# Performance work log

Measured on AMD Instinct MI355X. Metric: run time of the kernel, lower is better.

## Reference

```python
import jax, jax.numpy as jnp
import numpy as np

INPUT, UNITS, MOTOR, OUT = 1, 256, 64, 32
REM = UNITS - MOTOR
COMMAND = max(int(0.4 * REM), 1)   # 76
INTER = REM - COMMAND              # 116
B, L = 512, 1024
DIMS = [(INPUT, INTER), (INTER, COMMAND), (COMMAND, MOTOR)]


def setup_inputs() -> dict:
    rng = np.random.default_rng(0)
    inp = {}
    inp['dt'] = jnp.asarray(rng.random((B, L, INPUT)).astype(np.float32))
    inp['hx'] = jnp.asarray(rng.standard_normal((B, UNITS)).astype(np.float32))
    for i, (din, h) in enumerate(DIMS):
        c = din + h
        s = 1.0 / np.sqrt(c)
        for nm in ('W1', 'W2', 'Wa', 'Wb'):
            inp[f'l{i}_{nm}'] = jnp.asarray((rng.standard_normal((h, c)) * s).astype(np.float32))
        for nm in ('b1', 'b2', 'ba', 'bb'):
            inp[f'l{i}_{nm}'] = jnp.asarray((rng.standard_normal((h,)) * s).astype(np.float32))
        # NCP sparsity mask: random cross-layer connectivity (density ~0.5), dense recurrent block
        cross = (rng.random((h, din)) < 0.5).astype(np.int32)
        rec = np.ones((h, h), dtype=np.int32)
        inp[f'mask{i}'] = jnp.asarray(np.concatenate([cross, rec], axis=1))
    so = 1.0 / np.sqrt(MOTOR)
    inp['Wout'] = jnp.asarray((rng.standard_normal((OUT, MOTOR)) * so).astype(np.float32))
    inp['bout'] = jnp.asarray((rng.standard_normal((OUT,)) * so).astype(np.float32))
    return inp


def _cfc_cell(x, W1, W2, Wa, Wb, b1, b2, ba, bb, mask):
    # CfC 'default' mode, ts = 1.0 (CfC called without timespans; dt is the input signal)
    m = mask.astype(x.dtype)
    ff1 = jnp.tanh(x @ (W1 * m).T + b1)
    ff2 = jnp.tanh(x @ (W2 * m).T + b2)
    t_interp = jax.nn.sigmoid((x @ Wa.T + ba) + (x @ Wb.T + bb))
    return ff1 * (1.0 - t_interp) + t_interp * ff2


def _forward(dt, hx, params, masks, Wout, bout):
    # hx layout follows WiredCfCCell layer order: [inter, command, motor]
    h0, h1, h2 = jnp.split(hx, [INTER, INTER + COMMAND], axis=1)

    def step(carry, dt_t):
        h0, h1, h2 = carry
        h0 = _cfc_cell(jnp.concatenate([dt_t, h0], axis=-1), *params[0], masks[0])
        h1 = _cfc_cell(jnp.concatenate([h0, h1], axis=-1), *params[1], masks[1])
        h2 = _cfc_cell(jnp.concatenate([h1, h2], axis=-1), *params[2], masks[2])
        return (h0, h1, h2), h2

    _, ys = jax.lax.scan(step, (h0, h1, h2), jnp.swapaxes(dt, 0, 1))  # (L, B, MOTOR)
    readout = jnp.swapaxes(ys, 0, 1)  # (B, L, MOTOR)
    return readout @ Wout.T + bout    # (B, L, OUT)


def reference(dt, hx, l0_W1, l0_W2, l0_Wa, l0_Wb, l0_b1, l0_b2, l0_ba, l0_bb, l1_W1, l1_W2, l1_Wa, l1_Wb, l1_b1, l1_b2, l1_ba, l1_bb, l2_W1, l2_W2, l2_Wa, l2_Wb, l2_b1, l2_b2, l2_ba, l2_bb, mask0, mask1, mask2, Wout, bout):
    params = [
        (l0_W1, l0_W2, l0_Wa, l0_Wb, l0_b1, l0_b2, l0_ba, l0_bb),
        (l1_W1, l1_W2, l1_Wa, l1_Wb, l1_b1, l1_b2, l1_ba, l1_bb),
        (l2_W1, l2_W2, l2_Wa, l2_Wb, l2_b1, l2_b2, l2_ba, l2_bb),
    ]
    return _forward(dt, hx, params, (mask0, mask1, mask2), Wout, bout)
```

## Files before the change

### kernel.cpp

```cpp
#include <hip/hip_runtime.h>
#include <stdint.h>

typedef _Float16 f16;
typedef _Float16 h2v __attribute__((ext_vector_type(2)));
typedef _Float16 F16x4 __attribute__((ext_vector_type(4)));
typedef _Float16 F16x8 __attribute__((ext_vector_type(8)));
typedef float F32x4 __attribute__((ext_vector_type(4)));

#define MFMA16(a,b,c) __builtin_amdgcn_mfma_f32_16x16x32_f16((a),(b),(c),0,0,0)
#define S12f 2.8853900817779268f
#define SABf (-1.4426950408889634f)

static __device__ __forceinline__ float exp2f_b(float x){ return __builtin_amdgcn_exp2f(x); }

static __device__ __forceinline__ f16 cfc_act3(float p1,float p2,float ps){
  float E1=exp2f_b(p1), E2=exp2f_b(p2), es=exp2f_b(ps);
  float t1=E1+1.f, u=(E2+1.f)*(1.f+es);
  float num=u-(E2-E1);
  float r=__builtin_amdgcn_rcpf(t1*u);
  return (f16)(1.f-2.f*num*r);
}
static __device__ __forceinline__ int fidx(int k,int b){ return ((k>>3)<<7)+(b<<3)+(k&7); }

static __device__ __forceinline__ void tick_barrier(){
  asm volatile("s_waitcnt lgkmcnt(0)" ::: "memory");
  __builtin_amdgcn_s_barrier();
}

__global__ __launch_bounds__(256) void cfc_prep(
    const float* __restrict__ W10,const float* __restrict__ W20,const float* __restrict__ Wa0,const float* __restrict__ Wb0,
    const float* __restrict__ b10,const float* __restrict__ b20,const float* __restrict__ ba0,const float* __restrict__ bb0,
    const int* __restrict__ M0,
    const float* __restrict__ W11,const float* __restrict__ W21,const float* __restrict__ Wa1,const float* __restrict__ Wb1,
    const float* __restrict__ b11,const float* __restrict__ b21,const float* __restrict__ ba1,const float* __restrict__ bb1,
    const int* __restrict__ M1,
    const float* __restrict__ W12,const float* __restrict__ W22,const float* __restrict__ Wa2,const float* __restrict__ Wb2,
    const float* __restrict__ b12,const float* __restrict__ b22,const float* __restrict__ ba2,const float* __restrict__ bb2,
    const int* __restrict__ M2,
    const float* __restrict__ Wo, f16* __restrict__ ws)
{
  int idx=blockIdx.x*256+threadIdx.x;
  if(idx>=16704) return;
  int tile=idx>>6, lane=idx&63, ml=lane&15, grp=lane>>4;
  int lay,nb,m,kt,c,h;
  const float *w1,*w2,*wa,*wb,*c1,*c2,*ca,*cb; const int* M;
  if(tile<96){ lay=0; int u=tile; kt=u&3; int q=u>>2; m=q%3; nb=q/3; c=117; h=116;
    w1=W10;w2=W20;wa=Wa0;wb=Wb0;M=M0;c1=b10;c2=b20;ca=ba0;cb=bb0; }
  else if(tile<201){ lay=1; int u=tile-96; kt=u%7; int q=u/7; m=q%3; nb=q/3; c=192; h=76;
    w1=W11;w2=W21;wa=Wa1;wb=Wb1;M=M1;c1=b11;c2=b21;ca=ba1;cb=bb1; }
  else { lay=2; int u=tile-201; kt=u%5; int q=u/5; m=q%3; nb=q/3; c=140; h=64;
    w1=W12;w2=W22;wa=Wa2;wb=Wb2;M=M2;c1=b12;c2=b22;ca=ba2;cb=bb2; }
  int n=nb*16+ml;
  float sc=(m<2)?S12f:SABf;
  int k0=kt*32+grp*8;
  F16x8 fr;
  #pragma unroll
  for(int j=0;j<8;++j){
    int k=k0+j; float v=0.f; int col=-1;
    if(lay==0){       if(k<116) col=1+k; else if(k==124) col=0; else if(k==125) col=-2; }
    else if(lay==1){  if(k<116) col=k; else if(k>=128 && k<204) col=116+(k-128); else if(k==125) col=-2; }
    else {            if(k<76) col=k; else if(k>=96 && k<160) col=76+(k-96); else if(k==88) col=-2; }
    if(n<h){
      if(col>=0){
        if(m==0){ v=w1[n*c+col]*(float)M[n*c+col]; }
        else if(m==1){ v=w2[n*c+col]*(float)M[n*c+col]; }
        else { v=wa[n*c+col]+wb[n*c+col]; }
      } else if(col==-2){
        v=(m==0)?c1[n]:(m==1)?c2[n]:(ca[n]+cb[n]);
      }
    }
    fr[j]=(f16)(v*sc);
  }
  ((F16x8*)ws)[idx]=fr;
}

__global__ __launch_bounds__(1024,4) void cfc_main(
    const float* __restrict__ dtp, const float* __restrict__ hxp,
    const f16* __restrict__ ws, float* __restrict__ outp)
{
  const int tid=threadIdx.x, lane=tid&63, w=tid>>6;
  const int b_l=lane&15, g_l=lane>>4;
  const int gb0=blockIdx.x*16;

  __shared__ alignas(16) f16 H0[2][2048];
  __shared__ alignas(16) f16 H1[2][1536];
  __shared__ alignas(16) f16 H2[2][1024];
  __shared__ f16 DTS[16448];

  const F16x8* wsf=(const F16x8*)ws;
  F32x4 ZED; ZED[0]=0.f; ZED[1]=0.f; ZED[2]=0.f; ZED[3]=0.f;

  for(int i=tid;i<4096;i+=1024) ((f16*)H0)[i]=(f16)0.f;
  for(int i=tid;i<3072;i+=1024) ((f16*)H1)[i]=(f16)0.f;
  for(int i=tid;i<2048;i+=1024) ((f16*)H2)[i]=(f16)0.f;
  for(int i=tid;i<16448;i+=1024){
    int t=i>>4, b=i&15;
    DTS[i]=(t<1024)?(f16)dtp[(size_t)(gb0+b)*1024+t]:(f16)0.f;
  }
  __syncthreads();
  for(int i=tid;i<4096;i+=1024){ int b=i>>8,u=i&255; f16 v=(f16)hxp[(size_t)(gb0+b)*256+u];
    if(u<116){ H0[0][fidx(u,b)]=v; H0[1][fidx(u,b)]=v; }
    else if(u<192){ int n=u-116; H1[0][fidx(n,b)]=v; H1[1][fidx(n,b)]=v; }
    else { int n=u-192; H2[0][fidx(n,b)]=v; H2[1][fidx(n,b)]=v; }
  }
  if(tid<16){
    H0[1][fidx(124,tid)]=DTS[tid];
    H0[0][fidx(125,tid)]=(f16)1.f; H0[1][fidx(125,tid)]=(f16)1.f;
    H1[0][fidx(88,tid)]=(f16)1.f;  H1[1][fidx(88,tid)]=(f16)1.f;
  }
  __syncthreads();

  int type, nb=0;
  if(w==0){ type=0; }
  else if(w==1){type=1;nb=0;} else if(w==5){type=1;nb=1;} else if(w==2){type=1;nb=2;}
  else if(w==3){type=1;nb=3;} else if(w==7){type=1;nb=4;}
  else if(w==4){type=3;nb=0;} else if(w==6){type=3;nb=1;} else if(w==10){type=3;nb=2;}
  else { type=2; nb=(w==8)?0:(w==12)?1:(w==9)?2:(w==13)?3:(w==14)?4:(w==11)?5:6; }

  if(type==0){
    F16x8 wm0[3][4], wm2[3][5];
    #pragma unroll
    for(int m=0;m<3;++m){
      #pragma unroll
      for(int kt=0;kt<4;++kt) wm0[m][kt]=wsf[((7*3+m)*4+kt)*64+lane];
      #pragma unroll
      for(int kt=0;kt<5;++kt) wm2[m][kt]=wsf[(201+(3*3+m)*5+kt)*64+lane];
    }
    const int wk0=fidx(112+g_l*4,b_l);
    const int wk2=fidx(48+g_l*4,b_l);
#define MG_TICK(I_,P_) do{ \
      if((I_)<=1023){ \
        F16x8 Af0=((const F16x8*)H0[(P_)^1])[0*64+lane]; \
        F16x8 Af1=((const F16x8*)H0[(P_)^1])[1*64+lane]; \
        F16x8 Af2=((const F16x8*)H0[(P_)^1])[2*64+lane]; \
        F16x8 Af3=((const F16x8*)H0[(P_)^1])[3*64+lane]; \
        F32x4 a0=MFMA16(wm0[0][0],Af0,ZED), a1=MFMA16(wm0[1][0],Af0,ZED), a2=MFMA16(wm0[2][0],Af0,ZED); \
        a0=MFMA16(wm0[0][1],Af1,a0); a1=MFMA16(wm0[1][1],Af1,a1); a2=MFMA16(wm0[2][1],Af1,a2); \
        a0=MFMA16(wm0[0][2],Af2,a0); a1=MFMA16(wm0[1][2],Af2,a1); a2=MFMA16(wm0[2][2],Af2,a2); \
        a0=MFMA16(wm0[0][3],Af3,a0); a1=MFMA16(wm0[1][3],Af3,a1); a2=MFMA16(wm0[2][3],Af3,a2); \
        if(g_l==0){ \
          F16x4 v; v[0]=cfc_act3(a0[0],a1[0],a2[0]); v[1]=cfc_act3(a0[1],a1[1],a2[1]); \
          v[2]=cfc_act3(a0[2],a1[2],a2[2]); v[3]=cfc_act3(a0[3],a1[3],a2[3]); \
          *(F16x4*)&H0[P_][wk0]=v; } \
      } \
      if((I_)>=2 && (I_)<=1025){ \
        F16x8 Cf0=((const F16x8*)H1[(P_)^1])[0*64+lane]; \
        F16x8 Cf1=((const F16x8*)H1[(P_)^1])[1*64+lane]; \
        F16x8 Cf2=((const F16x8*)H1[(P_)^1])[2*64+lane]; \
        F16x8 Cf3=((const F16x8*)H2[(P_)^1])[0*64+lane]; \
        F16x8 Cf4=((const F16x8*)H2[(P_)^1])[1*64+lane]; \
        F32x4 c0=MFMA16(wm2[0][0],Cf0,ZED), c1=MFMA16(wm2[1][0],Cf0,ZED), c2=MFMA16(wm2[2][0],Cf0,ZED); \
        c0=MFMA16(wm2[0][1],Cf1,c0); c1=MFMA16(wm2[1][1],Cf1,c1); c2=MFMA16(wm2[2][1],Cf1,c2); \
        c0=MFMA16(wm2[0][2],Cf2,c0); c1=MFMA16(wm2[1][2],Cf2,c1); c2=MFMA16(wm2[2][2],Cf2,c2); \
        c0=MFMA16(wm2[0][3],Cf3,c0); c1=MFMA16(wm2[1][3],Cf3,c1); c2=MFMA16(wm2[2][3],Cf3,c2); \
        c0=MFMA16(wm2[0][4],Cf4,c0); c1=MFMA16(wm2[1][4],Cf4,c1); c2=MFMA16(wm2[2][4],Cf4,c2); \
        F16x4 v; v[0]=cfc_act3(c0[0],c1[0],c2[0]); v[1]=cfc_act3(c0[1],c1[1],c2[1]); \
        v[2]=cfc_act3(c0[2],c1[2],c2[2]); v[3]=cfc_act3(c0[3],c1[3],c2[3]); \
        *(F16x4*)&H2[P_][wk2]=v; \
      } }while(0)
    for(int I2=0;I2<1028;I2+=2){
      MG_TICK(I2,0);   tick_barrier();
      MG_TICK(I2+1,1); tick_barrier();
    }
#undef MG_TICK
  } else if(type==1){
    F16x8 wf[3][7];
    #pragma unroll
    for(int m=0;m<3;++m)
      #pragma unroll
      for(int kt=0;kt<7;++kt) wf[m][kt]=wsf[(96+(nb*3+m)*7+kt)*64+lane];
    const int wk=fidx(nb*16+g_l*4,b_l);
    const bool wr_ok=(nb<4)||(g_l<3);
#define L1_TICK(I_,P_) do{ \
      if((I_)>=1 && (I_)<=1024){ \
        F16x8 Af0=((const F16x8*)H0[(P_)^1])[0*64+lane]; \
        F16x8 Af1=((const F16x8*)H0[(P_)^1])[1*64+lane]; \
        F16x8 Af2=((const F16x8*)H0[(P_)^1])[2*64+lane]; \
        F16x8 Af3=((const F16x8*)H0[(P_)^1])[3*64+lane]; \
        F16x8 Hf0=((const F16x8*)H1[(P_)^1])[0*64+lane]; \
        F16x8 Hf1=((const F16x8*)H1[(P_)^1])[1*64+lane]; \
        F16x8 Hf2=((const F16x8*)H1[(P_)^1])[2*64+lane]; \
        F32x4 a0=MFMA16(wf[0][0],Af0,ZED), a1=MFMA16(wf[1][0],Af0,ZED), a2=MFMA16(wf[2][0],Af0,ZED); \
        a0=MFMA16(wf[0][1],Af1,a0); a1=MFMA16(wf[1][1],Af1,a1); a2=MFMA16(wf[2][1],Af1,a2); \
        a0=MFMA16(wf[0][2],Af2,a0); a1=MFMA16(wf[1][2],Af2,a1); a2=MFMA16(wf[2][2],Af2,a2); \
        a0=MFMA16(wf[0][3],Af3,a0); a1=MFMA16(wf[1][3],Af3,a1); a2=MFMA16(wf[2][3],Af3,a2); \
        a0=MFMA16(wf[0][4],Hf0,a0); a1=MFMA16(wf[1][4],Hf0,a1); a2=MFMA16(wf[2][4],Hf0,a2); \
        a0=MFMA16(wf[0][5],Hf1,a0); a1=MFMA16(wf[1][5],Hf1,a1); a2=MFMA16(wf[2][5],Hf1,a2); \
        a0=MFMA16(wf[0][6],Hf2,a0); a1=MFMA16(wf[1][6],Hf2,a1); a2=MFMA16(wf[2][6],Hf2,a2); \
        F16x4 v; v[0]=cfc_act3(a0[0],a1[0],a2[0]); v[1]=cfc_act3(a0[1],a1[1],a2[1]); \
        v[2]=cfc_act3(a0[2],a1[2],a2[2]); v[3]=cfc_act3(a0[3],a1[3],a2[3]); \
        if(wr_ok) *(F16x4*)&H1[P_][wk]=v; \
      } }while(0)
    for(int I2=0;I2<1028;I2+=2){
      L1_TICK(I2,0);   tick_barrier();
      L1_TICK(I2+1,1); tick_barrier();
    }
#undef L1_TICK
  } else if(type==2){
    F16x8 wf[3][4];
    #pragma unroll
    for(int m=0;m<3;++m)
      #pragma unroll
      for(int kt=0;kt<4;++kt) wf[m][kt]=wsf[((nb*3+m)*4+kt)*64+lane];
    const int wk=fidx(nb*16+g_l*4,b_l);
    const bool dost=(w==9)||(w==14);
    const int q=lane&7, bb=(lane>>3)+8*((w==9)?0:1);
    char* outPtr=(char*)outp + ((size_t)(gb0+bb)*1024)*128 + q*16;
#define L0_TICK(I_,P_) do{ \
      if((I_)<=1023){ \
        F16x8 Af0=((const F16x8*)H0[(P_)^1])[0*64+lane]; \
        F16x8 Af1=((const F16x8*)H0[(P_)^1])[1*64+lane]; \
        F16x8 Af2=((const F16x8*)H0[(P_)^1])[2*64+lane]; \
        F16x8 Af3=((const F16x8*)H0[(P_)^1])[3*64+lane]; \
        F32x4 a0=MFMA16(wf[0][0],Af0,ZED), a1=MFMA16(wf[1][0],Af0,ZED), a2=MFMA16(wf[2][0],Af0,ZED); \
        a0=MFMA16(wf[0][1],Af1,a0); a1=MFMA16(wf[1][1],Af1,a1); a2=MFMA16(wf[2][1],Af1,a2); \
        a0=MFMA16(wf[0][2],Af2,a0); a1=MFMA16(wf[1][2],Af2,a1); a2=MFMA16(wf[2][2],Af2,a2); \
        a0=MFMA16(wf[0][3],Af3,a0); a1=MFMA16(wf[1][3],Af3,a1); a2=MFMA16(wf[2][3],Af3,a2); \
        F16x4 v; v[0]=cfc_act3(a0[0],a1[0],a2[0]); v[1]=cfc_act3(a0[1],a1[1],a2[1]); \
        v[2]=cfc_act3(a0[2],a1[2],a2[2]); v[3]=cfc_act3(a0[3],a1[3],a2[3]); \
        *(F16x4*)&H0[P_][wk]=v; \
      } \
      if(dost && (I_)>=3 && (I_)<=1026){ \
        F16x8 sv=((const F16x8*)H2[(P_)^1])[q*16+bb]; \
        *(F16x8*)outPtr=sv; outPtr+=128; \
      } }while(0)
    for(int I2=0;I2<1028;I2+=2){
      L0_TICK(I2,0);   tick_barrier();
      L0_TICK(I2+1,1); tick_barrier();
    }
#undef L0_TICK
  } else {
    F16x8 wf[3][5];
    #pragma unroll
    for(int m=0;m<3;++m)
      #pragma unroll
      for(int kt=0;kt<5;++kt) wf[m][kt]=wsf[(201+(nb*3+m)*5+kt)*64+lane];
    const int wk=fidx(nb*16+g_l*4,b_l);
    const bool dodt=(w==6);
#define L2_TICK(I_,P_) do{ \
      if(dodt && lane<16 && (I_)<=1022) H0[P_][fidx(124,lane)]=DTS[((I_)+1)*16+lane]; \
      if((I_)>=2 && (I_)<=1025){ \
        F16x8 Cf0=((const F16x8*)H1[(P_)^1])[0*64+lane]; \
        F16x8 Cf1=((const F16x8*)H1[(P_)^1])[1*64+lane]; \
        F16x8 Cf2=((const F16x8*)H1[(P_)^1])[2*64+lane]; \
        F16x8 Cf3=((const F16x8*)H2[(P_)^1])[0*64+lane]; \
        F16x8 Cf4=((const F16x8*)H2[(P_)^1])[1*64+lane]; \
        F32x4 a0=MFMA16(wf[0][0],Cf0,ZED), a1=MFMA16(wf[1][0],Cf0,ZED), a2=MFMA16(wf[2][0],Cf0,ZED); \
        a0=MFMA16(wf[0][1],Cf1,a0); a1=MFMA16(wf[1][1],Cf1,a1); a2=MFMA16(wf[2][1],Cf1,a2); \
        a0=MFMA16(wf[0][2],Cf2,a0); a1=MFMA16(wf[1][2],Cf2,a1); a2=MFMA16(wf[2][2],Cf2,a2); \
        a0=MFMA16(wf[0][3],Cf3,a0); a1=MFMA16(wf[1][3],Cf3,a1); a2=MFMA16(wf[2][3],Cf3,a2); \
        a0=MFMA16(wf[0][4],Cf4,a0); a1=MFMA16(wf[1][4],Cf4,a1); a2=MFMA16(wf[2][4],Cf4,a2); \
        F16x4 v; v[0]=cfc_act3(a0[0],a1[0],a2[0]); v[1]=cfc_act3(a0[1],a1[1],a2[1]); \
        v[2]=cfc_act3(a0[2],a1[2],a2[2]); v[3]=cfc_act3(a0[3],a1[3],a2[3]); \
        *(F16x4*)&H2[P_][wk]=v; \
      } }while(0)
    for(int I2=0;I2<1028;I2+=2){
      L2_TICK(I2,0);   tick_barrier();
      L2_TICK(I2+1,1); tick_barrier();
    }
#undef L2_TICK
  }
}

__global__ __launch_bounds__(256) void cfc_ro(
    const float* __restrict__ Wo, const float* __restrict__ bo, float* __restrict__ outp)
{
  __shared__ h2v wT[1024];
  __shared__ float bs[32];
  int tid=threadIdx.x;
  for(int i=tid;i<1024;i+=256){ int kp=i>>5,o=i&31;
    h2v v; v[0]=(f16)Wo[o*64+2*kp]; v[1]=(f16)Wo[o*64+2*kp+1]; wT[i]=v; }
  if(tid<32) bs[tid]=bo[tid];
  __syncthreads();
  size_t s=(size_t)blockIdx.x*256+tid;
  float* slot=outp+s*32;
  h2v x[32];
  #pragma unroll
  for(int r=0;r<8;++r) ((F16x8*)x)[r]=((const F16x8*)slot)[r];
  float y[32];
  #pragma unroll
  for(int o=0;o<32;++o){
    float acc=bs[o];
    #pragma unroll
    for(int kp=0;kp<32;++kp) acc=__builtin_amdgcn_fdot2(x[kp],wT[kp*32+o],acc,false);
    y[o]=acc;
  }
  #pragma unroll
  for(int r=0;r<8;++r) ((float4*)slot)[r]=((const float4*)y)[r];
}

extern "C" void kernel_launch(void* const* d_in, const int* in_sizes, int n_in,
                              void* d_out, int out_size, void* d_ws, size_t ws_size,
                              hipStream_t stream)
{
  (void)in_sizes; (void)n_in; (void)out_size; (void)ws_size;
  f16* ws=(f16*)d_ws;
  cfc_prep<<<66,256,0,stream>>>(
    (const float*)d_in[2],(const float*)d_in[3],(const float*)d_in[4],(const float*)d_in[5],
    (const float*)d_in[6],(const float*)d_in[7],(const float*)d_in[8],(const float*)d_in[9],
    (const int*)d_in[10],
    (const float*)d_in[11],(const float*)d_in[12],(const float*)d_in[13],(const float*)d_in[14],
    (const float*)d_in[15],(const float*)d_in[16],(const float*)d_in[17],(const float*)d_in[18],
    (const int*)d_in[19],
    (const float*)d_in[20],(const float*)d_in[21],(const float*)d_in[22],(const float*)d_in[23],
    (const float*)d_in[24],(const float*)d_in[25],(const float*)d_in[26],(const float*)d_in[27],
    (const int*)d_in[28],
    (const float*)d_in[29], ws);
  cfc_main<<<32,1024,0,stream>>>(
    (const float*)d_in[0],(const float*)d_in[1], ws, (float*)d_out);
  cfc_ro<<<2048,256,0,stream>>>(
    (const float*)d_in[29],(const float*)d_in[30],(float*)d_out);
}
```

Before: 1.040 ms.

## Halve workgroup to 8 waves, each computing multiple output blocks per tick

The recurrent kernel moves from 16 waves per block to 8 waves, and the per-layer work is reassigned. Most waves now compute two or three 16-row output blocks per timestep, reusing the same loaded activation fragments across more MFMA chains. Fewer waves cut the cost of the two barriers per step and the redundant LDS fragment reads. In exchange, each wave has a longer serial MFMA and activation chain per tick and holds more weight registers, which may lengthen the critical path of each step.

Result: slower. 1.073 ms (+3.1%).

```diff
diff --git a/kernel.cpp b/kernel.cpp
--- a/kernel.cpp
+++ b/kernel.cpp
@@ -19,6 +19,12 @@
   float num=u-(E2-E1);
   float r=__builtin_amdgcn_rcpf(t1*u);
   return (f16)(1.f-2.f*num*r);
+}
+static __device__ __forceinline__ F16x4 pack_act3(F32x4 a0,F32x4 a1,F32x4 a2){
+  F16x4 v;
+  v[0]=cfc_act3(a0[0],a1[0],a2[0]); v[1]=cfc_act3(a0[1],a1[1],a2[1]);
+  v[2]=cfc_act3(a0[2],a1[2],a2[2]); v[3]=cfc_act3(a0[3],a1[3],a2[3]);
+  return v;
 }
 static __device__ __forceinline__ int fidx(int k,int b){ return ((k>>3)<<7)+(b<<3)+(k&7); }
 
@@ -74,7 +80,7 @@
   ((F16x8*)ws)[idx]=fr;
 }
 
-__global__ __launch_bounds__(1024,4) void cfc_main(
+__global__ __launch_bounds__(512,2) void cfc_main(
     const float* __restrict__ dtp, const float* __restrict__ hxp,
     const f16* __restrict__ ws, float* __restrict__ outp)
 {
@@ -90,15 +96,15 @@
   const F16x8* wsf=(const F16x8*)ws;
   F32x4 ZED; ZED[0]=0.f; ZED[1]=0.f; ZED[2]=0.f; ZED[3]=0.f;
 
-  for(int i=tid;i<4096;i+=1024) ((f16*)H0)[i]=(f16)0.f;
-  for(int i=tid;i<3072;i+=1024) ((f16*)H1)[i]=(f16)0.f;
-  for(int i=tid;i<2048;i+=1024) ((f16*)H2)[i]=(f16)0.f;
-  for(int i=tid;i<16448;i+=1024){
+  for(int i=tid;i<4096;i+=512) ((f16*)H0)[i]=(f16)0.f;
+  for(int i=tid;i<3072;i+=512) ((f16*)H1)[i]=(f16)0.f;
+  for(int i=tid;i<2048;i+=512) ((f16*)H2)[i]=(f16)0.f;
+  for(int i=tid;i<16448;i+=512){
     int t=i>>4, b=i&15;
     DTS[i]=(t<1024)?(f16)dtp[(size_t)(gb0+b)*1024+t]:(f16)0.f;
   }
   __syncthreads();
-  for(int i=tid;i<4096;i+=1024){ int b=i>>8,u=i&255; f16 v=(f16)hxp[(size_t)(gb0+b)*256+u];
+  for(int i=tid;i<4096;i+=512){ int b=i>>8,u=i&255; f16 v=(f16)hxp[(size_t)(gb0+b)*256+u];
     if(u<116){ H0[0][fidx(u,b)]=v; H0[1][fidx(u,b)]=v; }
     else if(u<192){ int n=u-116; H1[0][fidx(n,b)]=v; H1[1][fidx(n,b)]=v; }
     else { int n=u-192; H2[0][fidx(n,b)]=v; H2[1][fidx(n,b)]=v; }
@@ -110,68 +116,17 @@
   }
   __syncthreads();
 
-  int type, nb=0;
-  if(w==0){ type=0; }
-  else if(w==1){type=1;nb=0;} else if(w==5){type=1;nb=1;} else if(w==2){type=1;nb=2;}
-  else if(w==3){type=1;nb=3;} else if(w==7){type=1;nb=4;}
-  else if(w==4){type=3;nb=0;} else if(w==6){type=3;nb=1;} else if(w==10){type=3;nb=2;}
-  else { type=2; nb=(w==8)?0:(w==12)?1:(w==9)?2:(w==13)?3:(w==14)?4:(w==11)?5:6; }
-
-  if(type==0){
-    F16x8 wm0[3][4], wm2[3][5];
-    #pragma unroll
-    for(int m=0;m<3;++m){
-      #pragma unroll
-      for(int kt=0;kt<4;++kt) wm0[m][kt]=wsf[((7*3+m)*4+kt)*64+lane];
-      #pragma unroll
-      for(int kt=0;kt<5;++kt) wm2[m][kt]=wsf[(201+(3*3+m)*5+kt)*64+lane];
-    }
-    const int wk0=fidx(112+g_l*4,b_l);
-    const int wk2=fidx(48+g_l*4,b_l);
-#define MG_TICK(I_,P_) do{ \
-      if((I_)<=1023){ \
-        F16x8 Af0=((const F16x8*)H0[(P_)^1])[0*64+lane]; \
-        F16x8 Af1=((const F16x8*)H0[(P_)^1])[1*64+lane]; \
-        F16x8 Af2=((const F16x8*)H0[(P_)^1])[2*64+lane]; \
-        F16x8 Af3=((const F16x8*)H0[(P_)^1])[3*64+lane]; \
-        F32x4 a0=MFMA16(wm0[0][0],Af0,ZED), a1=MFMA16(wm0[1][0],Af0,ZED), a2=MFMA16(wm0[2][0],Af0,ZED); \
-        a0=MFMA16(wm0[0][1],Af1,a0); a1=MFMA16(wm0[1][1],Af1,a1); a2=MFMA16(wm0[2][1],Af1,a2); \
-        a0=MFMA16(wm0[0][2],Af2,a0); a1=MFMA16(wm0[1][2],Af2,a1); a2=MFMA16(wm0[2][2],Af2,a2); \
-        a0=MFMA16(wm0[0][3],Af3,a0); a1=MFMA16(wm0[1][3],Af3,a1); a2=MFMA16(wm0[2][3],Af3,a2); \
-        if(g_l==0){ \
-          F16x4 v; v[0]=cfc_act3(a0[0],a1[0],a2[0]); v[1]=cfc_act3(a0[1],a1[1],a2[1]); \
-          v[2]=cfc_act3(a0[2],a1[2],a2[2]); v[3]=cfc_act3(a0[3],a1[3],a2[3]); \
-          *(F16x4*)&H0[P_][wk0]=v; } \
-      } \
-      if((I_)>=2 && (I_)<=1025){ \
-        F16x8 Cf0=((const F16x8*)H1[(P_)^1])[0*64+lane]; \
-        F16x8 Cf1=((const F16x8*)H1[(P_)^1])[1*64+lane]; \
-        F16x8 Cf2=((const F16x8*)H1[(P_)^1])[2*64+lane]; \
-        F16x8 Cf3=((const F16x8*)H2[(P_)^1])[0*64+lane]; \
-        F16x8 Cf4=((const F16x8*)H2[(P_)^1])[1*64+lane]; \
-        F32x4 c0=MFMA16(wm2[0][0],Cf0,ZED), c1=MFMA16(wm2[1][0],Cf0,ZED), c2=MFMA16(wm2[2][0],Cf0,ZED); \
-        c0=MFMA16(wm2[0][1],Cf1,c0); c1=MFMA16(wm2[1][1],Cf1,c1); c2=MFMA16(wm2[2][1],Cf1,c2); \
-        c0=MFMA16(wm2[0][2],Cf2,c0); c1=MFMA16(wm2[1][2],Cf2,c1); c2=MFMA16(wm2[2][2],Cf2,c2); \
-        c0=MFMA16(wm2[0][3],Cf3,c0); c1=MFMA16(wm2[1][3],Cf3,c1); c2=MFMA16(wm2[2][3],Cf3,c2); \
-        c0=MFMA16(wm2[0][4],Cf4,c0); c1=MFMA16(wm2[1][4],Cf4,c1); c2=MFMA16(wm2[2][4],Cf4,c2); \
-        F16x4 v; v[0]=cfc_act3(c0[0],c1[0],c2[0]); v[1]=cfc_act3(c0[1],c1[1],c2[1]); \
-        v[2]=cfc_act3(c0[2],c1[2],c2[2]); v[3]=cfc_act3(c0[3],c1[3],c2[3]); \
-        *(F16x4*)&H2[P_][wk2]=v; \
-      } }while(0)
-    for(int I2=0;I2<1028;I2+=2){
-      MG_TICK(I2,0);   tick_barrier();
-      MG_TICK(I2+1,1); tick_barrier();
-    }
-#undef MG_TICK
-  } else if(type==1){
-    F16x8 wf[3][7];
-    #pragma unroll
-    for(int m=0;m<3;++m)
-      #pragma unroll
-      for(int kt=0;kt<7;++kt) wf[m][kt]=wsf[(96+(nb*3+m)*7+kt)*64+lane];
-    const int wk=fidx(nb*16+g_l*4,b_l);
-    const bool wr_ok=(nb<4)||(g_l<3);
-#define L1_TICK(I_,P_) do{ \
+  if(w<2){
+    const int NB=2*w;
+    F16x8 wf[6][7];
+    #pragma unroll
+    for(int u=0;u<2;++u)
+      #pragma unroll
+      for(int m=0;m<3;++m)
+        #pragma unroll
+        for(int kt=0;kt<7;++kt) wf[u*3+m][kt]=wsf[(96+((NB+u)*3+m)*7+kt)*64+lane];
+    const int wka=fidx((NB+0)*16+g_l*4,b_l), wkb=fidx((NB+1)*16+g_l*4,b_l);
+#define L1P_TICK(I_,P_) do{ \
       if((I_)>=1 && (I_)<=1024){ \
         F16x8 Af0=((const F16x8*)H0[(P_)^1])[0*64+lane]; \
         F16x8 Af1=((const F16x8*)H0[(P_)^1])[1*64+lane]; \
@@ -181,33 +136,44 @@
         F16x8 Hf1=((const F16x8*)H1[(P_)^1])[1*64+lane]; \
         F16x8 Hf2=((const F16x8*)H1[(P_)^1])[2*64+lane]; \
         F32x4 a0=MFMA16(wf[0][0],Af0,ZED), a1=MFMA16(wf[1][0],Af0,ZED), a2=MFMA16(wf[2][0],Af0,ZED); \
+        F32x4 b0=MFMA16(wf[3][0],Af0,ZED), b1=MFMA16(wf[4][0],Af0,ZED), b2=MFMA16(wf[5][0],Af0,ZED); \
         a0=MFMA16(wf[0][1],Af1,a0); a1=MFMA16(wf[1][1],Af1,a1); a2=MFMA16(wf[2][1],Af1,a2); \
+        b0=MFMA16(wf[3][1],Af1,b0); b1=MFMA16(wf[4][1],Af1,b1); b2=MFMA16(wf[5][1],Af1,b2); \
         a0=MFMA16(wf[0][2],Af2,a0); a1=MFMA16(wf[1][2],Af2,a1); a2=MFMA16(wf[2][2],Af2,a2); \
+        b0=MFMA16(wf[3][2],Af2,b0); b1=MFMA16(wf[4][2],Af2,b1); b2=MFMA16(wf[5][2],Af2,b2); \
         a0=MFMA16(wf[0][3],Af3,a0); a1=MFMA16(wf[1][3],Af3,a1); a2=MFMA16(wf[2][3],Af3,a2); \
+        b0=MFMA16(wf[3][3],Af3,b0); b1=MFMA16(wf[4][3],Af3,b1); b2=MFMA16(wf[5][3],Af3,b2); \
         a0=MFMA16(wf[0][4],Hf0,a0); a1=MFMA16(wf[1][4],Hf0,a1); a2=MFMA16(wf[2][4],Hf0,a2); \
+        b0=MFMA16(wf[3][4],Hf0,b0); b1=MFMA16(wf[4][4],Hf0,b1); b2=MFMA16(wf[5][4],Hf0,b2); \
         a0=MFMA16(wf[0][5],Hf1,a0); a1=MFMA16(wf[1][5],Hf1,a1); a2=MFMA16(wf[2][5],Hf1,a2); \
+        b0=MFMA16(wf[3][5],Hf1,b0); b1=MFMA16(wf[4][5],Hf1,b1); b2=MFMA16(wf[5][5],Hf1,b2); \
         a0=MFMA16(wf[0][6],Hf2,a0); a1=MFMA16(wf[1][6],Hf2,a1); a2=MFMA16(wf[2][6],Hf2,a2); \
-        F16x4 v; v[0]=cfc_act3(a0[0],a1[0],a2[0]); v[1]=cfc_act3(a0[1],a1[1],a2[1]); \
-        v[2]=cfc_act3(a0[2],a1[2],a2[2]); v[3]=cfc_act3(a0[3],a1[3],a2[3]); \
-        if(wr_ok) *(F16x4*)&H1[P_][wk]=v; \
+        b0=MFMA16(wf[3][6],Hf2,b0); b1=MFMA16(wf[4][6],Hf2,b1); b2=MFMA16(wf[5][6],Hf2,b2); \
+        *(F16x4*)&H1[P_][wka]=pack_act3(a0,a1,a2); \
+        *(F16x4*)&H1[P_][wkb]=pack_act3(b0,b1,b2); \
       } }while(0)
     for(int I2=0;I2<1028;I2+=2){
-      L1_TICK(I2,0);   tick_barrier();
-      L1_TICK(I2+1,1); tick_barrier();
-    }
-#undef L1_TICK
-  } else if(type==2){
-    F16x8 wf[3][4];
-    #pragma unroll
-    for(int m=0;m<3;++m)
-      #pragma unroll
-      for(int kt=0;kt<4;++kt) wf[m][kt]=wsf[((nb*3+m)*4+kt)*64+lane];
-    const int wk=fidx(nb*16+g_l*4,b_l);
-    const bool dost=(w==9)||(w==14);
-    const int q=lane&7, bb=(lane>>3)+8*((w==9)?0:1);
-    char* outPtr=(char*)outp + ((size_t)(gb0+bb)*1024)*128 + q*16;
-#define L0_TICK(I_,P_) do{ \
-      if((I_)<=1023){ \
+      L1P_TICK(I2,0);   tick_barrier();
+      L1P_TICK(I2+1,1); tick_barrier();
+    }
+#undef L1P_TICK
+  } else if(w==2){
+    F16x8 wf[3][7], wc[3][5];
+    #pragma unroll
+    for(int m=0;m<3;++m){
+      #pragma unroll
+      for(int kt=0;kt<7;++kt) wf[m][kt]=wsf[(96+(4*3+m)*7+kt)*64+lane];
+      #pragma unroll
+      for(int kt=0;kt<5;++kt) wc[m][kt]=wsf[(201+(0*3+m)*5+kt)*64+lane];
+    }
+    const int wk1=fidx(64+g_l*4,b_l);
+    const int wk2=fidx(0+g_l*4,b_l);
+    const bool wr1=(g_l<3);
+#define MIX_TICK(I_,P_) do{ \
+      F16x8 Hf0=((const F16x8*)H1[(P_)^1])[0*64+lane]; \
+      F16x8 Hf1=((const F16x8*)H1[(P_)^1])[1*64+lane]; \
+      F16x8 Hf2=((const F16x8*)H1[(P_)^1])[2*64+lane]; \
+      if((I_)>=1 && (I_)<=1024){ \
         F16x8 Af0=((const F16x8*)H0[(P_)^1])[0*64+lane]; \
         F16x8 Af1=((const F16x8*)H0[(P_)^1])[1*64+lane]; \
         F16x8 Af2=((const F16x8*)H0[(P_)^1])[2*64+lane]; \
@@ -216,49 +182,109 @@
         a0=MFMA16(wf[0][1],Af1,a0); a1=MFMA16(wf[1][1],Af1,a1); a2=MFMA16(wf[2][1],Af1,a2); \
         a0=MFMA16(wf[0][2],Af2,a0); a1=MFMA16(wf[1][2],Af2,a1); a2=MFMA16(wf[2][2],Af2,a2); \
         a0=MFMA16(wf[0][3],Af3,a0); a1=MFMA16(wf[1][3],Af3,a1); a2=MFMA16(wf[2][3],Af3,a2); \
-        F16x4 v; v[0]=cfc_act3(a0[0],a1[0],a2[0]); v[1]=cfc_act3(a0[1],a1[1],a2[1]); \
-        v[2]=cfc_act3(a0[2],a1[2],a2[2]); v[3]=cfc_act3(a0[3],a1[3],a2[3]); \
-        *(F16x4*)&H0[P_][wk]=v; \
+        a0=MFMA16(wf[0][4],Hf0,a0); a1=MFMA16(wf[1][4],Hf0,a1); a2=MFMA16(wf[2][4],Hf0,a2); \
+        a0=MFMA16(wf[0][5],Hf1,a0); a1=MFMA16(wf[1][5],Hf1,a1); a2=MFMA16(wf[2][5],Hf1,a2); \
+        a0=MFMA16(wf[0][6],Hf2,a0); a1=MFMA16(wf[1][6],Hf2,a1); a2=MFMA16(wf[2][6],Hf2,a2); \
+        F16x4 v=pack_act3(a0,a1,a2); \
+        if(wr1) *(F16x4*)&H1[P_][wk1]=v; \
+      } \
+      if((I_)>=2 && (I_)<=1025){ \
+        F16x8 Gf0=((const F16x8*)H2[(P_)^1])[0*64+lane]; \
+        F16x8 Gf1=((const F16x8*)H2[(P_)^1])[1*64+lane]; \
+        F32x4 c0=MFMA16(wc[0][0],Hf0,ZED), c1=MFMA16(wc[1][0],Hf0,ZED), c2=MFMA16(wc[2][0],Hf0,ZED); \
+        c0=MFMA16(wc[0][1],Hf1,c0); c1=MFMA16(wc[1][1],Hf1,c1); c2=MFMA16(wc[2][1],Hf1,c2); \
+        c0=MFMA16(wc[0][2],Hf2,c0); c1=MFMA16(wc[1][2],Hf2,c1); c2=MFMA16(wc[2][2],Hf2,c2); \
+        c0=MFMA16(wc[0][3],Gf0,c0); c1=MFMA16(wc[1][3],Gf0,c1); c2=MFMA16(wc[2][3],Gf0,c2); \
+        c0=MFMA16(wc[0][4],Gf1,c0); c1=MFMA16(wc[1][4],Gf1,c1); c2=MFMA16(wc[2][4],Gf1,c2); \
+        *(F16x4*)&H2[P_][wk2]=pack_act3(c0,c1,c2); \
+      } }while(0)
+    for(int I2=0;I2<1028;I2+=2){
+      MIX_TICK(I2,0);   tick_barrier();
+      MIX_TICK(I2+1,1); tick_barrier();
+    }
+#undef MIX_TICK
+  } else if(w==3){
+    F16x8 wc[9][5];
+    #pragma unroll
+    for(int u=0;u<3;++u)
+      #pragma unroll
+      for(int m=0;m<3;++m)
+        #pragma unroll
+        for(int kt=0;kt<5;++kt) wc[u*3+m][kt]=wsf[(201+((1+u)*3+m)*5+kt)*64+lane];
+    const int wka=fidx(16+g_l*4,b_l), wkb=fidx(32+g_l*4,b_l), wkc=fidx(48+g_l*4,b_l);
+#define L2T_TICK(I_,P_) do{ \
+      if((I_)>=2 && (I_)<=1025){ \
+        F16x8 Hf0=((const F16x8*)H1[(P_)^1])[0*64+lane]; \
+        F16x8 Hf1=((const F16x8*)H1[(P_)^1])[1*64+lane]; \
+        F16x8 Hf2=((const F16x8*)H1[(P_)^1])[2*64+lane]; \
+        F16x8 Gf0=((const F16x8*)H2[(P_)^1])[0*64+lane]; \
+        F16x8 Gf1=((const F16x8*)H2[(P_)^1])[1*64+lane]; \
+        F32x4 a0=MFMA16(wc[0][0],Hf0,ZED), a1=MFMA16(wc[1][0],Hf0,ZED), a2=MFMA16(wc[2][0],Hf0,ZED); \
+        F32x4 b0=MFMA16(wc[3][0],Hf0,ZED), b1=MFMA16(wc[4][0],Hf0,ZED), b2=MFMA16(wc[5][0],Hf0,ZED); \
+        F32x4 c0=MFMA16(wc[6][0],Hf0,ZED), c1=MFMA16(wc[7][0],Hf0,ZED), c2=MFMA16(wc[8][0],Hf0,ZED); \
+        a0=MFMA16(wc[0][1],Hf1,a0); a1=MFMA16(wc[1][1],Hf1,a1); a2=MFMA16(wc[2][1],Hf1,a2); \
+        b0=MFMA16(wc[3][1],Hf1,b0); b1=MFMA16(wc[4][1],Hf1,b1); b2=MFMA16(wc[5][1],Hf1,b2); \
+        c0=MFMA16(wc[6][1],Hf1,c0); c1=MFMA16(wc[7][1],Hf1,c1); c2=MFMA16(wc[8][1],Hf1,c2); \
+        a0=MFMA16(wc[0][2],Hf2,a0); a1=MFMA16(wc[1][2],Hf2,a1); a2=MFMA16(wc[2][2],Hf2,a2); \
+        b0=MFMA16(wc[3][2],Hf2,b0); b1=MFMA16(wc[4][2],Hf2,b1); b2=MFMA16(wc[5][2],Hf2,b2); \
+        c0=MFMA16(wc[6][2],Hf2,c0); c1=MFMA16(wc[7][2],Hf2,c1); c2=MFMA16(wc[8][2],Hf2,c2); \
+        a0=MFMA16(wc[0][3],Gf0,a0); a1=MFMA16(wc[1][3],Gf0,a1); a2=MFMA16(wc[2][3],Gf0,a2); \
+        b0=MFMA16(wc[3][3],Gf0,b0); b1=MFMA16(wc[4][3],Gf0,b1); b2=MFMA16(wc[5][3],Gf0,b2); \
+        c0=MFMA16(wc[6][3],Gf0,c0); c1=MFMA16(wc[7][3],Gf0,c1); c2=MFMA16(wc[8][3],Gf0,c2); \
+        a0=MFMA16(wc[0][4],Gf1,a0); a1=MFMA16(wc[1][4],Gf1,a1); a2=MFMA16(wc[2][4],Gf1,a2); \
+        b0=MFMA16(wc[3][4],Gf1,b0); b1=MFMA16(wc[4][4],Gf1,b1); b2=MFMA16(wc[5][4],Gf1,b2); \
+        c0=MFMA16(wc[6][4],Gf1,c0); c1=MFMA16(wc[7][4],Gf1,c1); c2=MFMA16(wc[8][4],Gf1,c2); \
+        *(F16x4*)&H2[P_][wka]=pack_act3(a0,a1,a2); \
+        *(F16x4*)&H2[P_][wkb]=pack_act3(b0,b1,b2); \
+        *(F16x4*)&H2[P_][wkc]=pack_act3(c0,c1,c2); \
+      } }while(0)
+    for(int I2=0;I2<1028;I2+=2){
+      L2T_TICK(I2,0);   tick_barrier();
+      L2T_TICK(I2+1,1); tick_barrier();
+    }
+#undef L2T_TICK
+  } else {
+    const int NB=2*(w-4);
+    F16x8 wf[6][4];
+    #pragma unroll
+    for(int u=0;u<2;++u)
+      #pragma unroll
+      for(int m=0;m<3;++m)
+        #pragma unroll
+        for(int kt=0;kt<4;++kt) wf[u*3+m][kt]=wsf[(((NB+u)*3+m)*4+kt)*64+lane];
+    const int wka=fidx((NB+0)*16+g_l*4,b_l), wkb=fidx((NB+1)*16+g_l*4,b_l);
+    const bool wrb=(w<7)||(g_l==0);
+    const bool dost=(w==4)||(w==5);
+    const bool dodt=(w==6);
+    const int q=lane&7, bb=(lane>>3)+8*(w-4);
+    char* outPtr=(char*)outp + ((size_t)(gb0+(bb&15))*1024)*128 + q*16;
+#define L0P_TICK(I_,P_) do{ \
+      if(dodt && lane<16 && (I_)<=1022) H0[P_][fidx(124,lane)]=DTS[((I_)+1)*16+lane]; \
+      if((I_)<=1023){ \
+        F16x8 Af0=((const F16x8*)H0[(P_)^1])[0*64+lane]; \
+        F16x8 Af1=((const F16x8*)H0[(P_)^1])[1*64+lane]; \
+        F16x8 Af2=((const F16x8*)H0[(P_)^1])[2*64+lane]; \
+        F16x8 Af3=((const F16x8*)H0[(P_)^1])[3*64+lane]; \
+        F32x4 a0=MFMA16(wf[0][0],Af0,ZED), a1=MFMA16(wf[1][0],Af0,ZED), a2=MFMA16(wf[2][0],Af0,ZED); \
+        F32x4 b0=MFMA16(wf[3][0],Af0,ZED), b1=MFMA16(wf[4][0],Af0,ZED), b2=MFMA16(wf[5][0],Af0,ZED); \
+        a0=MFMA16(wf[0][1],Af1,a0); a1=MFMA16(wf[1][1],Af1,a1); a2=MFMA16(wf[2][1],Af1,a2); \
+        b0=MFMA16(wf[3][1],Af1,b0); b1=MFMA16(wf[4][1],Af1,b1); b2=MFMA16(wf[5][1],Af1,b2); \
+        a0=MFMA16(wf[0][2],Af2,a0); a1=MFMA16(wf[1][2],Af2,a1); a2=MFMA16(wf[2][2],Af2,a2); \
+        b0=MFMA16(wf[3][2],Af2,b0); b1=MFMA16(wf[4][2],Af2,b1); b2=MFMA16(wf[5][2],Af2,b2); \
+        a0=MFMA16(wf[0][3],Af3,a0); a1=MFMA16(wf[1][3],Af3,a1); a2=MFMA16(wf[2][3],Af3,a2); \
+        b0=MFMA16(wf[3][3],Af3,b0); b1=MFMA16(wf[4][3],Af3,b1); b2=MFMA16(wf[5][3],Af3,b2); \
+        *(F16x4*)&H0[P_][wka]=pack_act3(a0,a1,a2); \
+        if(wrb) *(F16x4*)&H0[P_][wkb]=pack_act3(b0,b1,b2); \
       } \
       if(dost && (I_)>=3 && (I_)<=1026){ \
-        F16x8 sv=((const F16x8*)H2[(P_)^1])[q*16+bb]; \
+        F16x8 sv=((const F16x8*)H2[(P_)^1])[q*16+(bb&15)]; \
         *(F16x8*)outPtr=sv; outPtr+=128; \
       } }while(0)
     for(int I2=0;I2<1028;I2+=2){
-      L0_TICK(I2,0);   tick_barrier();
-      L0_TICK(I2+1,1); tick_barrier();
-    }
-#undef L0_TICK
-  } else {
-    F16x8 wf[3][5];
-    #pragma unroll
-    for(int m=0;m<3;++m)
-      #pragma unroll
-      for(int kt=0;kt<5;++kt) wf[m][kt]=wsf[(201+(nb*3+m)*5+kt)*64+lane];
-    const int wk=fidx(nb*16+g_l*4,b_l);
-    const bool dodt=(w==6);
-#define L2_TICK(I_,P_) do{ \
-      if(dodt && lane<16 && (I_)<=1022) H0[P_][fidx(124,lane)]=DTS[((I_)+1)*16+lane]; \
-      if((I_)>=2 && (I_)<=1025){ \
-        F16x8 Cf0=((const F16x8*)H1[(P_)^1])[0*64+lane]; \
-        F16x8 Cf1=((const F16x8*)H1[(P_)^1])[1*64+lane]; \
-        F16x8 Cf2=((const F16x8*)H1[(P_)^1])[2*64+lane]; \
-        F16x8 Cf3=((const F16x8*)H2[(P_)^1])[0*64+lane]; \
-        F16x8 Cf4=((const F16x8*)H2[(P_)^1])[1*64+lane]; \
-        F32x4 a0=MFMA16(wf[0][0],Cf0,ZED), a1=MFMA16(wf[1][0],Cf0,ZED), a2=MFMA16(wf[2][0],Cf0,ZED); \
-        a0=MFMA16(wf[0][1],Cf1,a0); a1=MFMA16(wf[1][1],Cf1,a1); a2=MFMA16(wf[2][1],Cf1,a2); \
-        a0=MFMA16(wf[0][2],Cf2,a0); a1=MFMA16(wf[1][2],Cf2,a1); a2=MFMA16(wf[2][2],Cf2,a2); \
-        a0=MFMA16(wf[0][3],Cf3,a0); a1=MFMA16(wf[1][3],Cf3,a1); a2=MFMA16(wf[2][3],Cf3,a2); \
-        a0=MFMA16(wf[0][4],Cf4,a0); a1=MFMA16(wf[1][4],Cf4,a1); a2=MFMA16(wf[2][4],Cf4,a2); \
-        F16x4 v; v[0]=cfc_act3(a0[0],a1[0],a2[0]); v[1]=cfc_act3(a0[1],a1[1],a2[1]); \
-        v[2]=cfc_act3(a0[2],a1[2],a2[2]); v[3]=cfc_act3(a0[3],a1[3],a2[3]); \
-        *(F16x4*)&H2[P_][wk]=v; \
-      } }while(0)
-    for(int I2=0;I2<1028;I2+=2){
-      L2_TICK(I2,0);   tick_barrier();
-      L2_TICK(I2+1,1); tick_barrier();
-    }
-#undef L2_TICK
+      L0P_TICK(I2,0);   tick_barrier();
+      L0P_TICK(I2+1,1); tick_barrier();
+    }
+#undef L0P_TICK
   }
 }
 
@@ -306,7 +332,7 @@
     (const float*)d_in[24],(const float*)d_in[25],(const float*)d_in[26],(const float*)d_in[27],
     (const int*)d_in[28],
     (const float*)d_in[29], ws);
-  cfc_main<<<32,1024,0,stream>>>(
+  cfc_main<<<32,512,0,stream>>>(
     (const float*)d_in[0],(const float*)d_in[1], ws, (float*)d_out);
   cfc_ro<<<2048,256,0,stream>>>(
     (const float*)d_in[29],(const float*)d_in[30],(float*)d_out);
```
